# Kernel tuning notes

Measured on AMD Instinct MI355X. Metric: run time of the kernel, lower is better.

The kernel has to match this reference:

```python
import jax, jax.numpy as jnp
import numpy as np
import math

# ---- GPT-OSS attention config (gpt-oss-20b) ----
HIDDEN = 2880
HEAD_DIM = 64
N_Q_HEADS = 64
N_KV_HEADS = 8
GROUP = N_Q_HEADS // N_KV_HEADS  # 8
WINDOW = 128                      # sliding window (keys in (q-128, q])
ROPE_BASE = 150000.0
SCALING_FACTOR = 32.0
NTK_ALPHA = 1.0
NTK_BETA = 32.0
INIT_CTX = 4096
Q_SIZE = N_Q_HEADS * HEAD_DIM     # 4096
KV_SIZE = N_KV_HEADS * HEAD_DIM   # 512
SM_SCALE = HEAD_DIM ** -0.5


def _yarn_inv_freq_and_concentration():
    """YaRN-scaled inverse frequencies (matches GptOssRotaryEmbedding)."""
    d_half = HEAD_DIM / 2
    freq = ROPE_BASE ** (np.arange(0, HEAD_DIM, 2, dtype=np.float32) / HEAD_DIM)
    concentration = 0.1 * math.log(SCALING_FACTOR) + 1.0
    low = d_half * math.log(INIT_CTX / (NTK_BETA * 2 * math.pi)) / math.log(ROPE_BASE)
    high = d_half * math.log(INIT_CTX / (NTK_ALPHA * 2 * math.pi)) / math.log(ROPE_BASE)
    interpolation = 1.0 / (SCALING_FACTOR * freq)
    extrapolation = 1.0 / freq
    ramp = (np.arange(d_half, dtype=np.float32) - low) / (high - low)
    mask = 1.0 - np.clip(ramp, 0.0, 1.0)
    inv_freq = interpolation * (1.0 - mask) + extrapolation * mask
    return jnp.asarray(inv_freq, jnp.float32), jnp.float32(concentration)

_INV_FREQ, _CONC = _yarn_inv_freq_and_concentration()


def _apply_rope(x, cos, sin):
    # x: [n, h, d]; cos/sin: [n, d/2] (neox style: rotate halves)
    d2 = HEAD_DIM // 2
    x1, x2 = x[..., :d2], x[..., d2:]
    c, s = cos[:, None, :], sin[:, None, :]
    return jnp.concatenate([x1 * c - x2 * s, x2 * c + x1 * s], axis=-1)


def setup_inputs() -> dict:
    key = jax.random.key(0)
    ks = jax.random.split(key, 6)
    n = 8192
    return {
        "hidden_states": jax.random.normal(ks[0], (n, HIDDEN), jnp.float32),
        "position_ids": jnp.arange(n, dtype=jnp.int32),
        "qkv_w": jax.random.normal(ks[1], (Q_SIZE + 2 * KV_SIZE, HIDDEN), jnp.float32) * (HIDDEN ** -0.5),
        "qkv_b": jax.random.normal(ks[2], (Q_SIZE + 2 * KV_SIZE,), jnp.float32) * 0.02,
        "o_w": jax.random.normal(ks[3], (HIDDEN, Q_SIZE), jnp.float32) * (Q_SIZE ** -0.5),
        "o_b": jax.random.normal(ks[4], (HIDDEN,), jnp.float32) * 0.02,
        "sinks": jax.random.normal(ks[5], (N_Q_HEADS,), jnp.float32),
    }


def reference(hidden_states, position_ids, qkv_w, qkv_b, o_w, o_b, sinks):
    n = hidden_states.shape[0]
    W = WINDOW
    nb = n // W  # n must be a multiple of the window (8192 / 128 = 64)

    # QKV projection
    qkv = hidden_states @ qkv_w.T + qkv_b
    q = qkv[:, :Q_SIZE].reshape(n, N_Q_HEADS, HEAD_DIM)
    k = qkv[:, Q_SIZE:Q_SIZE + KV_SIZE].reshape(n, N_KV_HEADS, HEAD_DIM)
    v = qkv[:, Q_SIZE + KV_SIZE:].reshape(n, N_KV_HEADS, HEAD_DIM)

    # RoPE (YaRN, neox)
    angles = position_ids.astype(jnp.float32)[:, None] * _INV_FREQ[None, :]
    cos = jnp.cos(angles) * _CONC
    sin = jnp.sin(angles) * _CONC
    q = _apply_rope(q, cos, sin)
    k = _apply_rope(k, cos, sin)

    # Blocked sliding-window attention: each W-block of queries attends to
    # [previous block, own block] keys (window=W keys incl. self).
    qb = (q * SM_SCALE).reshape(nb, W, N_KV_HEADS, GROUP, HEAD_DIM)
    kb = k.reshape(nb, W, N_KV_HEADS, HEAD_DIM)
    vb = v.reshape(nb, W, N_KV_HEADS, HEAD_DIM)
    k2 = jnp.concatenate([jnp.concatenate([jnp.zeros_like(kb[:1]), kb[:-1]], 0), kb], axis=1)  # [nb,2W,Hk,d]
    v2 = jnp.concatenate([jnp.concatenate([jnp.zeros_like(vb[:1]), vb[:-1]], 0), vb], axis=1)

    # scores: [nb, Hk, G, W, 2W]
    scores = jnp.einsum('bqgjd,bkgd->bgjqk', qb, k2)

    # mask: key global idx = (b-1)*W + j; need 0 <= q-k <= W-1 and k >= 0
    i = jnp.arange(W)[:, None]
    j = jnp.arange(2 * W)[None, :]
    mrel = (j >= i + 1) & (j <= i + W)                       # [W, 2W]
    first = (jnp.arange(nb)[:, None, None] > 0) | (j >= W)   # [nb, 1|W, 2W]
    mask = (mrel[None] & first)[:, None, None, :, :]          # [nb,1,1,W,2W]

    neg_inf = jnp.float32(-jnp.inf)
    s = jnp.where(mask, scores, neg_inf)
    sink = sinks.reshape(N_KV_HEADS, GROUP)[None, :, :, None]  # [1,Hk,G,1]
    m = jnp.maximum(jnp.max(s, axis=-1), sink)                  # [nb,Hk,G,W]
    e = jnp.exp(s - m[..., None])
    denom = e.sum(axis=-1) + jnp.exp(sink - m)                  # sink adds to denominator only
    p = e / denom[..., None]

    out = jnp.einsum('bgjqk,bkgd->bqgjd', p, v2).reshape(n, Q_SIZE)
    return out @ o_w.T + o_b
```

## Files before the change

kernel.cpp:

```cpp
#include <hip/hip_runtime.h>
#include <math.h>
#include <stdint.h>

typedef float  f32x4  __attribute__((ext_vector_type(4)));
typedef __bf16 bf16x8 __attribute__((ext_vector_type(8)));
typedef __bf16 bf16x4 __attribute__((ext_vector_type(4)));

#define MFMA16(a, b, c) __builtin_amdgcn_mfma_f32_16x16x32_bf16(a, b, c, 0, 0, 0)

__device__ __forceinline__ void async16(const void* g, void* l) {
  __builtin_amdgcn_global_load_lds((__attribute__((address_space(1))) void*)g,
                                   (__attribute__((address_space(3))) void*)l,
                                   16, 0, 0);
}

__global__ __launch_bounds__(256) void cast_f32_to_bf16(const float* __restrict__ in,
                                                        __bf16* __restrict__ out, int n) {
  int idx = (blockIdx.x * 256 + threadIdx.x) * 4;
  if (idx + 3 < n) {
    float4 v = *(const float4*)(in + idx);
    bf16x4 o;
    o[0] = (__bf16)v.x; o[1] = (__bf16)v.y; o[2] = (__bf16)v.z; o[3] = (__bf16)v.w;
    *(bf16x4*)(out + idx) = o;
  }
}

__global__ __launch_bounds__(256) void rope_table_kernel(const int* __restrict__ pos_ids,
                                                         float2* __restrict__ tab, int total) {
  int idx = blockIdx.x * 256 + threadIdx.x;
  if (idx >= total) return;
  int p = idx >> 5, d = idx & 31;
  float posf = (float)pos_ids[p];
  float ex = (float)(2 * d) * (1.0f / 64.0f);
  float freq = powf(150000.0f, ex);
  float inv_scaled = 1.0f / (32.0f * freq);
  float inv_plain = 1.0f / freq;
  float lr = logf(150000.0f);
  const float TWO_PI = 6.28318530717958647692f;
  float low  = 32.0f * logf(4096.0f / (32.0f * TWO_PI)) / lr;
  float high = 32.0f * logf(4096.0f / TWO_PI) / lr;
  float ramp = ((float)d - low) / (high - low);
  ramp = fminf(fmaxf(ramp, 0.0f), 1.0f);
  float maskv = 1.0f - ramp;
  float inv_freq = inv_scaled * (1.0f - maskv) + inv_plain * maskv;
  float conc = 0.1f * logf(32.0f) + 1.0f;
  float ang = posf * inv_freq;
  float s, c;
  sincosf(ang, &s, &c);
  tab[idx] = make_float2(c * conc, s * conc);
}

template <typename OutT, bool DO_ROPE>
__global__ __launch_bounds__(256) void gemm_bt(const __bf16* __restrict__ A,
                                               const __bf16* __restrict__ B,
                                               const float* __restrict__ bias,
                                               OutT* __restrict__ C,
                                               const float2* __restrict__ tab,
                                               int M, int N, int K) {
  __shared__ __align__(16) __bf16 As[128 * 32];
  __shared__ __align__(16) __bf16 Bs[128 * 32];
  const int tid = threadIdx.x;
  const int wv = tid >> 6;
  const int ln = tid & 63;
  const int l16 = ln & 15;
  const int quad = ln >> 4;
  const int nTN = (N + 127) >> 7;
  int bid = (int)blockIdx.x;
  int nwg = (int)gridDim.x;
  int swz = bid;
  if ((nwg & 7) == 0) {
    int cpx = nwg >> 3;
    swz = (bid & 7) * cpx + (bid >> 3);
  }
  const int brow = swz / nTN;
  const int bcol = swz % nTN;
  const int row0 = brow << 7, col0 = bcol << 7;
  const int wr = wv >> 1, wc = wv & 1;
  const int srow = ln >> 2;
  const int scol = (((ln & 3) ^ ((ln >> 3) & 3)) * 8);
  const int rsw = (l16 >> 1) & 3;

  f32x4 acc[4][4];
#pragma unroll
  for (int t = 0; t < 4; t++)
#pragma unroll
    for (int u = 0; u < 4; u++) acc[t][u] = (f32x4){0.f, 0.f, 0.f, 0.f};

  for (int k0 = 0; k0 < K; k0 += 32) {
#pragma unroll
    for (int s = wv; s < 8; s += 4) {
      int rA = row0 + s * 16 + srow;
      int rB = col0 + s * 16 + srow;
      if (rB > N - 1) rB = N - 1;
      async16(A + (size_t)rA * K + k0 + scol, (char*)As + s * 1024);
      async16(B + (size_t)rB * K + k0 + scol, (char*)Bs + s * 1024);
    }
    __syncthreads();
    bf16x8 af[4], bfr[4];
#pragma unroll
    for (int t = 0; t < 4; t++)
      af[t] = *(const bf16x8*)&As[(wr * 64 + t * 16 + l16) * 32 + (quad ^ rsw) * 8];
#pragma unroll
    for (int u = 0; u < 4; u++)
      bfr[u] = *(const bf16x8*)&Bs[(wc * 64 + u * 16 + l16) * 32 + (quad ^ rsw) * 8];
#pragma unroll
    for (int t = 0; t < 4; t++)
#pragma unroll
      for (int u = 0; u < 4; u++)
        acc[t][u] = MFMA16(af[t], bfr[u], acc[t][u]);
    __syncthreads();
  }

  const int hh = (col0 + wc * 64) >> 6;
  if (DO_ROPE && hh < 72) {
    const float scale = hh < 64 ? 0.125f : 1.0f;
    float bv[4];
#pragma unroll
    for (int u = 0; u < 4; u++) bv[u] = bias[col0 + wc * 64 + u * 16 + l16];
#pragma unroll
    for (int t = 0; t < 4; t++) {
      int rowb = row0 + wr * 64 + t * 16 + quad * 4;
#pragma unroll
      for (int r = 0; r < 4; r++) {
        int row = rowb + r;
#pragma unroll
        for (int u = 0; u < 2; u++) {
          float2 cs = tab[row * 32 + u * 16 + l16];
          float x1 = acc[t][u][r] + bv[u];
          float x2 = acc[t][u + 2][r] + bv[u + 2];
          C[(size_t)row * N + col0 + wc * 64 + u * 16 + l16] =
              (OutT)((x1 * cs.x - x2 * cs.y) * scale);
          C[(size_t)row * N + col0 + wc * 64 + (u + 2) * 16 + l16] =
              (OutT)((x2 * cs.x + x1 * cs.y) * scale);
        }
      }
    }
  } else {
#pragma unroll
    for (int u = 0; u < 4; u++) {
      int col = col0 + wc * 64 + u * 16 + l16;
      if (col < N) {
        float bv = bias[col];
#pragma unroll
        for (int t = 0; t < 4; t++) {
          int row = row0 + wr * 64 + t * 16 + quad * 4;
#pragma unroll
          for (int r = 0; r < 4; r++)
            C[(size_t)(row + r) * N + col] = (OutT)(acc[t][u][r] + bv);
        }
      }
    }
  }
}

__global__ __launch_bounds__(256) void attn_kernel(const __bf16* __restrict__ qkv,
                                                   const float* __restrict__ sinks,
                                                   __bf16* __restrict__ out) {
  __shared__ __align__(16) __bf16 vT_s[64 * 264];
  __shared__ __align__(16) __bf16 p_s[64 * 136];
  const int tid = threadIdx.x;
  const int bh = blockIdx.x >> 1;
  const int qh = blockIdx.x & 1;
  const int b = bh >> 3;
  const int h = bh & 7;
  const int wv = tid >> 6;
  const int ln = tid & 63;
  const int l16 = ln & 15;
  const int quad = ln >> 4;

  for (int c = tid; c < 2048; c += 256) {
    int key = c >> 3, dc = c & 7;
    int vpos = b * 128 + key - 128;
    bf16x8 vv = {};
    if (vpos >= 0)
      vv = *(const bf16x8*)(qkv + (size_t)vpos * 5120 + 4608 + h * 64 + dc * 8);
    int keysw = key ^ ((dc & 3) << 3);
#pragma unroll
    for (int l2 = 0; l2 < 8; l2++)
      vT_s[(dc * 8 + l2) * 264 + keysw] = vv[l2];
  }
  __syncthreads();

#pragma unroll 1
  for (int pass = 0; pass < 8; pass++) {
    int g = qh * 4 + (pass >> 1);
    int i0 = (pass & 1) * 64 + wv * 16;
    int head = h * 8 + g;
    float sink = sinks[head];

    size_t qbase = (size_t)(b * 128 + i0 + l16) * 5120 + head * 64;
    bf16x8 aq0 = *(const bf16x8*)(qkv + qbase + quad * 8);
    bf16x8 aq1 = *(const bf16x8*)(qkv + qbase + 32 + quad * 8);

    f32x4 sc[16];
#pragma unroll
    for (int ct = 0; ct < 16; ct++) {
      int key = ct * 16 + l16;
      int kpos = b * 128 + key - 128;
      if (kpos < 0) kpos = 0;
      const __bf16* kp = qkv + (size_t)kpos * 5120 + 4096 + h * 64;
      bf16x8 kb0 = *(const bf16x8*)(kp + quad * 8);
      bf16x8 kb1 = *(const bf16x8*)(kp + 32 + quad * 8);
      f32x4 z = (f32x4){0.f, 0.f, 0.f, 0.f};
      __builtin_amdgcn_s_setprio(1);
      z = MFMA16(aq0, kb0, z);
      z = MFMA16(aq1, kb1, z);
      __builtin_amdgcn_s_setprio(0);
      sc[ct] = z;
    }

    float mx[4] = {-INFINITY, -INFINITY, -INFINITY, -INFINITY};
#pragma unroll
    for (int ct = 0; ct < 16; ct++) {
      int j = ct * 16 + l16;
#pragma unroll
      for (int r = 0; r < 4; r++) {
        int i = i0 + quad * 4 + r;
        bool valid = (j >= i + 1) && (j <= i + 128) && (b > 0 || j >= 128);
        float s = valid ? sc[ct][r] : -INFINITY;
        sc[ct][r] = s;
        mx[r] = fmaxf(mx[r], s);
      }
    }
#pragma unroll
    for (int off = 1; off < 16; off <<= 1)
#pragma unroll
      for (int r = 0; r < 4; r++)
        mx[r] = fmaxf(mx[r], __shfl_xor(mx[r], off));
#pragma unroll
    for (int r = 0; r < 4; r++) mx[r] = fmaxf(mx[r], sink);

    float sum[4] = {0.f, 0.f, 0.f, 0.f};
#pragma unroll
    for (int ct = 0; ct < 16; ct++)
#pragma unroll
      for (int r = 0; r < 4; r++) {
        float e = __expf(sc[ct][r] - mx[r]);
        sc[ct][r] = e;
        sum[r] += e;
      }
#pragma unroll
    for (int off = 1; off < 16; off <<= 1)
#pragma unroll
      for (int r = 0; r < 4; r++)
        sum[r] += __shfl_xor(sum[r], off);

    f32x4 o[4];
#pragma unroll
    for (int dt = 0; dt < 4; dt++) o[dt] = (f32x4){0.f, 0.f, 0.f, 0.f};
#pragma unroll 1
    for (int kh = 0; kh < 2; kh++) {
#pragma unroll
      for (int ct = 0; ct < 8; ct++)
#pragma unroll
        for (int r = 0; r < 4; r++)
          p_s[(wv * 16 + quad * 4 + r) * 136 + ct * 16 + l16] = (__bf16)sc[kh * 8 + ct][r];
#pragma unroll
      for (int ks = 0; ks < 4; ks++) {
        bf16x8 pa = *(const bf16x8*)&p_s[(wv * 16 + l16) * 136 + ks * 32 + quad * 8];
        __builtin_amdgcn_s_setprio(1);
#pragma unroll
        for (int dt = 0; dt < 4; dt++) {
          int sw = ((dt * 2 + (l16 >> 3)) & 3) << 3;
          bf16x8 vb = *(const bf16x8*)&vT_s[(dt * 16 + l16) * 264 +
                                            ((kh * 128 + ks * 32 + quad * 8) ^ sw)];
          o[dt] = MFMA16(pa, vb, o[dt]);
        }
        __builtin_amdgcn_s_setprio(0);
      }
    }

#pragma unroll
    for (int r = 0; r < 4; r++) {
      float rd = 1.0f / (sum[r] + __expf(sink - mx[r]));
      int posn = b * 128 + i0 + quad * 4 + r;
      size_t obase = (size_t)posn * 4096 + head * 64;
#pragma unroll
      for (int dt = 0; dt < 4; dt++)
        out[obase + dt * 16 + l16] = (__bf16)(o[dt][r] * rd);
    }
  }
}

extern "C" void kernel_launch(void* const* d_in, const int* in_sizes, int n_in,
                              void* d_out, int out_size, void* d_ws, size_t ws_size,
                              hipStream_t stream) {
  (void)in_sizes; (void)n_in; (void)out_size; (void)ws_size;
  const float* hs     = (const float*)d_in[0];
  const int*   pos    = (const int*)d_in[1];
  const float* qkv_w  = (const float*)d_in[2];
  const float* qkv_b  = (const float*)d_in[3];
  const float* o_w    = (const float*)d_in[4];
  const float* o_b    = (const float*)d_in[5];
  const float* sinks  = (const float*)d_in[6];
  float* outp = (float*)d_out;
  char* ws = (char*)d_ws;

  const size_t O_QKV = 0;
  const size_t O_ATT = 83886080;
  const size_t O_TAB = 131072000;
  const size_t O_W   = 150994944;
  __bf16* qkvb = (__bf16*)(ws + O_QKV);
  __bf16* hsb  = (__bf16*)(ws + O_ATT);
  __bf16* attn = (__bf16*)(ws + O_ATT);
  float2* tab  = (float2*)(ws + O_TAB);
  __bf16* wb   = (__bf16*)(ws + O_W);

  cast_f32_to_bf16<<<23040, 256, 0, stream>>>(hs, hsb, 8192 * 2880);
  cast_f32_to_bf16<<<14400, 256, 0, stream>>>(qkv_w, wb, 5120 * 2880);
  rope_table_kernel<<<1024, 256, 0, stream>>>(pos, tab, 8192 * 32);
  gemm_bt<__bf16, true><<<64 * 40, 256, 0, stream>>>(hsb, wb, qkv_b, qkvb, tab,
                                                     8192, 5120, 2880);
  cast_f32_to_bf16<<<11520, 256, 0, stream>>>(o_w, wb, 2880 * 4096);
  attn_kernel<<<1024, 256, 0, stream>>>(qkvb, sinks, attn);
  gemm_bt<float, false><<<64 * 23, 256, 0, stream>>>(attn, wb, o_b, outp, nullptr,
                                                     8192, 2880, 4096);
}
```

Baseline: 961.5 us.

## Replace 128x128 GEMM with 256x256 tile, 8-wave, multi-buffered async pipeline

Both GEMMs now use a 256x256 output tile computed by 512 threads (8 waves, each 128x64). The K loop runs in 64-wide steps over a 4-slot LDS ring of async global->LDS loads, with explicit vmcnt waits, barriers, and setprio so loads overlap MFMA phases. The goal is more data reuse per tile and hidden memory latency compared with the single-buffered 128x128 loop that synchronised twice per 32-K step. The cost is 128KB of LDS, large accumulator register pressure, and hand-managed waitcnt logic that can break if the compiler reorders loads.

```diff
diff --git a/kernel.cpp b/kernel.cpp
--- a/kernel.cpp
+++ b/kernel.cpp
@@ -51,20 +51,25 @@
 }
 
 template <typename OutT, bool DO_ROPE>
-__global__ __launch_bounds__(256) void gemm_bt(const __bf16* __restrict__ A,
-                                               const __bf16* __restrict__ B,
-                                               const float* __restrict__ bias,
-                                               OutT* __restrict__ C,
-                                               const float2* __restrict__ tab,
-                                               int M, int N, int K) {
-  __shared__ __align__(16) __bf16 As[128 * 32];
-  __shared__ __align__(16) __bf16 Bs[128 * 32];
+__global__ __launch_bounds__(512, 2) void gemm256(const __bf16* __restrict__ A,
+                                                  const __bf16* __restrict__ B,
+                                                  const float* __restrict__ bias,
+                                                  OutT* __restrict__ C,
+                                                  const float2* __restrict__ tab,
+                                                  int M, int N, int K) {
+  __shared__ __align__(16) __bf16 lds_all[65536];
+  __bf16* Asl = lds_all;
+  __bf16* Bsl = lds_all + 32768;
+
   const int tid = threadIdx.x;
-  const int wv = tid >> 6;
-  const int ln = tid & 63;
+  const int wv  = tid >> 6;
+  const int ln  = tid & 63;
   const int l16 = ln & 15;
   const int quad = ln >> 4;
-  const int nTN = (N + 127) >> 7;
+  const int wr = wv >> 2;
+  const int wc = wv & 3;
+
+  const int nTN = (N + 255) >> 8;
   int bid = (int)blockIdx.x;
   int nwg = (int)gridDim.x;
   int swz = bid;
@@ -74,42 +79,120 @@
   }
   const int brow = swz / nTN;
   const int bcol = swz % nTN;
-  const int row0 = brow << 7, col0 = bcol << 7;
-  const int wr = wv >> 1, wc = wv & 1;
-  const int srow = ln >> 2;
-  const int scol = (((ln & 3) ^ ((ln >> 3) & 3)) * 8);
-  const int rsw = (l16 >> 1) & 3;
-
-  f32x4 acc[4][4];
-#pragma unroll
-  for (int t = 0; t < 4; t++)
+  const int row0 = brow << 8, col0 = bcol << 8;
+
+  const int rsw  = (l16 >> 1) & 3;
+  const int aoff = (wr * 128 + l16) * 32 + ((quad ^ rsw) * 8);
+  const int boff = (wc * 64 + l16) * 32 + ((quad ^ rsw) * 8);
+
+  const int srow = tid >> 2;
+  const int skq  = (tid & 3) ^ ((tid >> 3) & 3);
+
+  auto stA = [&](int t_, int kh) {
+    const __bf16* s = A + (size_t)(row0 + srow) * K + t_ * 64 + kh * 32 + skq * 8;
+    char* d = (char*)Asl + (((2 * t_ + kh) & 3) << 14) + (wv << 10);
+    async16(s, d);
+    async16(s + (size_t)128 * K, d + 8192);
+  };
+  auto stB = [&](int t_, int kh) {
+    int r0 = col0 + srow;       if (r0 > N - 1) r0 = N - 1;
+    int r1 = col0 + srow + 128; if (r1 > N - 1) r1 = N - 1;
+    const int kb = t_ * 64 + kh * 32 + skq * 8;
+    char* d = (char*)Bsl + (((2 * t_ + kh) & 3) << 14) + (wv << 10);
+    async16(B + (size_t)r0 * K + kb, d);
+    async16(B + (size_t)r1 * K + kb, d + 8192);
+  };
+
+  f32x4 acc[8][4];
+#pragma unroll
+  for (int t = 0; t < 8; t++)
 #pragma unroll
     for (int u = 0; u < 4; u++) acc[t][u] = (f32x4){0.f, 0.f, 0.f, 0.f};
 
-  for (int k0 = 0; k0 < K; k0 += 32) {
-#pragma unroll
-    for (int s = wv; s < 8; s += 4) {
-      int rA = row0 + s * 16 + srow;
-      int rB = col0 + s * 16 + srow;
-      if (rB > N - 1) rB = N - 1;
-      async16(A + (size_t)rA * K + k0 + scol, (char*)As + s * 1024);
-      async16(B + (size_t)rB * K + k0 + scol, (char*)Bs + s * 1024);
-    }
-    __syncthreads();
-    bf16x8 af[4], bfr[4];
-#pragma unroll
-    for (int t = 0; t < 4; t++)
-      af[t] = *(const bf16x8*)&As[(wr * 64 + t * 16 + l16) * 32 + (quad ^ rsw) * 8];
-#pragma unroll
-    for (int u = 0; u < 4; u++)
-      bfr[u] = *(const bf16x8*)&Bs[(wc * 64 + u * 16 + l16) * 32 + (quad ^ rsw) * 8];
-#pragma unroll
-    for (int t = 0; t < 4; t++)
-#pragma unroll
-      for (int u = 0; u < 4; u++)
-        acc[t][u] = MFMA16(af[t], bfr[u], acc[t][u]);
-    __syncthreads();
-  }
+  const int nt = K >> 6;
+
+  stA(0, 0); stB(0, 0); stA(0, 1); stB(0, 1);
+  if (nt > 1) {
+    stA(1, 0); stB(1, 0); stA(1, 1); stB(1, 1);
+    asm volatile("s_waitcnt vmcnt(4)" ::: "memory");
+  } else {
+    asm volatile("s_waitcnt vmcnt(0)" ::: "memory");
+  }
+  __builtin_amdgcn_s_barrier();
+
+#define PHASE_TAIL()                                      \
+  __builtin_amdgcn_s_barrier();                           \
+  asm volatile("s_waitcnt lgkmcnt(0)" ::: "memory");      \
+  __builtin_amdgcn_sched_barrier(0);                      \
+  __builtin_amdgcn_s_setprio(1);
+
+#define PHASE_END()                                       \
+  __builtin_amdgcn_s_setprio(0);                          \
+  __builtin_amdgcn_s_barrier();
+
+#pragma unroll 1
+  for (int t = 0; t < nt; ++t) {
+    const __bf16* As0 = Asl + (((2 * t) & 3) << 13);
+    const __bf16* Bs0 = Bsl + (((2 * t) & 3) << 13);
+    const __bf16* As1 = Asl + (((2 * t + 1) & 3) << 13);
+    const __bf16* Bs1 = Bsl + (((2 * t + 1) & 3) << 13);
+    bf16x8 a[8], b0, b1;
+
+#pragma unroll
+    for (int tt = 0; tt < 8; ++tt) a[tt] = *(const bf16x8*)(As0 + aoff + tt * 512);
+    b0 = *(const bf16x8*)(Bs0 + boff);
+    b1 = *(const bf16x8*)(Bs0 + boff + 512);
+    if (t >= 1 && t + 1 < nt) stA(t + 1, 1);
+    PHASE_TAIL();
+#pragma unroll
+    for (int tt = 0; tt < 8; ++tt) {
+      acc[tt][0] = MFMA16(a[tt], b0, acc[tt][0]);
+      acc[tt][1] = MFMA16(a[tt], b1, acc[tt][1]);
+    }
+    PHASE_END();
+
+    b0 = *(const bf16x8*)(Bs0 + boff + 1024);
+    b1 = *(const bf16x8*)(Bs0 + boff + 1536);
+    if (t >= 1 && t + 1 < nt) stB(t + 1, 1);
+    PHASE_TAIL();
+#pragma unroll
+    for (int tt = 0; tt < 8; ++tt) {
+      acc[tt][2] = MFMA16(a[tt], b0, acc[tt][2]);
+      acc[tt][3] = MFMA16(a[tt], b1, acc[tt][3]);
+    }
+    PHASE_END();
+
+#pragma unroll
+    for (int tt = 0; tt < 8; ++tt) a[tt] = *(const bf16x8*)(As1 + aoff + tt * 512);
+    b0 = *(const bf16x8*)(Bs1 + boff);
+    b1 = *(const bf16x8*)(Bs1 + boff + 512);
+    if (t + 2 < nt) stA(t + 2, 0);
+    PHASE_TAIL();
+#pragma unroll
+    for (int tt = 0; tt < 8; ++tt) {
+      acc[tt][0] = MFMA16(a[tt], b0, acc[tt][0]);
+      acc[tt][1] = MFMA16(a[tt], b1, acc[tt][1]);
+    }
+    PHASE_END();
+
+    b0 = *(const bf16x8*)(Bs1 + boff + 1024);
+    b1 = *(const bf16x8*)(Bs1 + boff + 1536);
+    if (t + 2 < nt) {
+      stB(t + 2, 0);
+      asm volatile("s_waitcnt vmcnt(4)" ::: "memory");
+    } else {
+      asm volatile("s_waitcnt vmcnt(0)" ::: "memory");
+    }
+    PHASE_TAIL();
+#pragma unroll
+    for (int tt = 0; tt < 8; ++tt) {
+      acc[tt][2] = MFMA16(a[tt], b0, acc[tt][2]);
+      acc[tt][3] = MFMA16(a[tt], b1, acc[tt][3]);
+    }
+    PHASE_END();
+  }
+#undef PHASE_TAIL
+#undef PHASE_END
 
   const int hh = (col0 + wc * 64) >> 6;
   if (DO_ROPE && hh < 72) {
@@ -118,16 +201,16 @@
 #pragma unroll
     for (int u = 0; u < 4; u++) bv[u] = bias[col0 + wc * 64 + u * 16 + l16];
 #pragma unroll
-    for (int t = 0; t < 4; t++) {
-      int rowb = row0 + wr * 64 + t * 16 + quad * 4;
+    for (int tt = 0; tt < 8; ++tt) {
+      int rowb = row0 + wr * 128 + tt * 16 + quad * 4;
 #pragma unroll
       for (int r = 0; r < 4; r++) {
         int row = rowb + r;
 #pragma unroll
         for (int u = 0; u < 2; u++) {
           float2 cs = tab[row * 32 + u * 16 + l16];
-          float x1 = acc[t][u][r] + bv[u];
-          float x2 = acc[t][u + 2][r] + bv[u + 2];
+          float x1 = acc[tt][u][r] + bv[u];
+          float x2 = acc[tt][u + 2][r] + bv[u + 2];
           C[(size_t)row * N + col0 + wc * 64 + u * 16 + l16] =
               (OutT)((x1 * cs.x - x2 * cs.y) * scale);
           C[(size_t)row * N + col0 + wc * 64 + (u + 2) * 16 + l16] =
@@ -142,11 +225,11 @@
       if (col < N) {
         float bv = bias[col];
 #pragma unroll
-        for (int t = 0; t < 4; t++) {
-          int row = row0 + wr * 64 + t * 16 + quad * 4;
+        for (int tt = 0; tt < 8; ++tt) {
+          int row = row0 + wr * 128 + tt * 16 + quad * 4;
 #pragma unroll
           for (int r = 0; r < 4; r++)
-            C[(size_t)(row + r) * N + col] = (OutT)(acc[t][u][r] + bv);
+            C[(size_t)(row + r) * N + col] = (OutT)(acc[tt][u][r] + bv);
         }
       }
     }
@@ -309,10 +392,10 @@
   cast_f32_to_bf16<<<23040, 256, 0, stream>>>(hs, hsb, 8192 * 2880);
   cast_f32_to_bf16<<<14400, 256, 0, stream>>>(qkv_w, wb, 5120 * 2880);
   rope_table_kernel<<<1024, 256, 0, stream>>>(pos, tab, 8192 * 32);
-  gemm_bt<__bf16, true><<<64 * 40, 256, 0, stream>>>(hsb, wb, qkv_b, qkvb, tab,
-                                                     8192, 5120, 2880);
+  gemm256<__bf16, true><<<640, 512, 0, stream>>>(hsb, wb, qkv_b, qkvb, tab,
+                                                 8192, 5120, 2880);
   cast_f32_to_bf16<<<11520, 256, 0, stream>>>(o_w, wb, 2880 * 4096);
   attn_kernel<<<1024, 256, 0, stream>>>(qkvb, sinks, attn);
-  gemm_bt<float, false><<<64 * 23, 256, 0, stream>>>(attn, wb, o_b, outp, nullptr,
-                                                     8192, 2880, 4096);
-}
+  gemm256<float, false><<<384, 512, 0, stream>>>(attn, wb, o_b, outp, nullptr,
+                                                 8192, 2880, 4096);
+}
```

New measurement: 926.4 us. 3.7% less time.
